# Optimization experiments

Hardware: AMD Instinct MI355X
Metric: run time of the kernel (lower is better)

The kernel has to match this reference:

```python
import jax, jax.numpy as jnp
import numpy as np

E, H, K = 768, 512, 8  # word_emb_size, nhidden, nhead
B, NA, NC = 32, 64, 64


def setup_inputs() -> dict:
    key = jax.random.key(0)
    ks = jax.random.split(key, 8)
    w = lambda k, shape: (jax.random.normal(k, shape, jnp.float32) * 0.02)
    return {
        'he_anchor': jax.random.normal(ks[0], (B, NA, E), jnp.float32),
        'he_pos': jax.random.normal(ks[1], (B, NC, E), jnp.float32),
        'he_neg': jax.random.uniform(ks[2], (B,), jnp.float32),  # SBERT target scores
        'Wa': w(ks[3], (H, E)), 'ba': jnp.zeros((H,), jnp.float32),
        'Wc': w(ks[4], (H, E)), 'bc': jnp.zeros((H,), jnp.float32),
        'Watt': w(ks[5], (K, H)), 'batt': jnp.zeros((K,), jnp.float32),
        'Wscore': w(ks[6], (1, K * H)), 'bscore': jnp.zeros((1,), jnp.float32),
    }


def _score(ha, hc, Wa, ba, Wc, bc, Watt, batt, Wscore, bscore):
    b, na, _ = ha.shape
    A = ha @ Wa.T + ba  # [B,Na,H]  (a2h)
    C = hc @ Wc.T + bc  # [B,Nc,H]  (c2h)
    # self_mul[b,i,j,h] = A[b,i,h]*C[b,j,h]; att logits = h2att(self_mul)
    logits = jnp.einsum('bih,bjh,kh->bkij', A, C, Watt) + batt[None, :, None, None]
    att = jax.nn.softmax(logits.reshape(b, K, -1), axis=-1).reshape(logits.shape)  # [B,K,Na,Nc]
    # per-head bilinear: out[b,k,h] = sum_ij A[b,i,h] * att[b,k,i,j] * C[b,j,h]
    out = jnp.einsum('bih,bkij,bjh->bkh', A, att, C)  # [B,K,H], head-major like torch cat
    score = out.reshape(b, K * H) @ Wscore.T + bscore  # [B,1]
    return score, att


def reference(he_anchor, he_pos, he_neg, Wa, ba, Wc, bc, Watt, batt, Wscore, bscore):
    score_p, att_map = _score(he_anchor, he_pos, Wa, ba, Wc, bc, Watt, batt, Wscore, bscore)
    score_bert = he_neg.reshape(-1, 1)
    loss = jnp.mean((score_p - score_bert) ** 2)  # nn.MSELoss
    return score_p, loss, att_map
```

## Files before the change

kernel.cpp:

```cpp
#include <hip/hip_runtime.h>

#define E_DIM 768

typedef __attribute__((ext_vector_type(8))) short bf16x8;
typedef __attribute__((ext_vector_type(4))) float f32x4;

__device__ __forceinline__ unsigned short f2bf(float f) {
    union { float f; unsigned int u; } v; v.f = f;
    unsigned int u = v.u;
    return (unsigned short)((u + 0x7FFFu + ((u >> 16) & 1u)) >> 16);
}
__device__ __forceinline__ float bfu_lo(unsigned int u) {
    union { unsigned int u; float f; } v; v.u = u << 16; return v.f;
}
__device__ __forceinline__ float bfu_hi(unsigned int u) {
    union { unsigned int u; float f; } v; v.u = u & 0xFFFF0000u; return v.f;
}
__device__ __forceinline__ unsigned int cvt_pk_bf16(float lo, float hi) {
    unsigned int u;
    asm("v_cvt_pk_bf16_f32 %0, %1, %2" : "=v"(u) : "v"(lo), "v"(hi));
    return u;
}

__global__ __launch_bounds__(256) void k_proj_mfma(
    const float* __restrict__ he_a, const float* __restrict__ Wa, const float* __restrict__ ba,
    const float* __restrict__ he_p, const float* __restrict__ Wc, const float* __restrict__ bc,
    unsigned short* __restrict__ dsts)
{
    __shared__ unsigned short Xs[128 * 40];
    __shared__ unsigned short Wl[64 * 40];
    int bid = blockIdx.x;
    int which = bid >> 7;
    int loc = bid & 127;
    int mbase = (loc >> 3) * 128;
    int hbase = (loc & 7) * 64;
    const float* Xg = which ? he_p : he_a;
    const float* Wg = which ? Wc : Wa;
    const float* bias = which ? bc : ba;
    int t = threadIdx.x;
    int lane = t & 63, w = t >> 6;
    int wr = w >> 1, wc = w & 1;

    float4 xr4[4];
    float4 wr4[2];
#pragma unroll
    for (int it = 0; it < 4; ++it) {
        int idx = t + it * 256; int row = idx >> 3, c4 = idx & 7;
        xr4[it] = *(const float4*)(Xg + (size_t)(mbase + row) * E_DIM + c4 * 4);
    }
#pragma unroll
    for (int it = 0; it < 2; ++it) {
        int idx = t + it * 256; int row = idx >> 3, c4 = idx & 7;
        wr4[it] = *(const float4*)(Wg + (size_t)(hbase + row) * E_DIM + c4 * 4);
    }

    f32x4 acc[4][2] = {};
    for (int kt = 0; kt < 24; ++kt) {
        __syncthreads();
#pragma unroll
        for (int it = 0; it < 4; ++it) {
            int idx = t + it * 256; int row = idx >> 3, c4 = idx & 7;
            uint2 u = make_uint2(cvt_pk_bf16(xr4[it].x, xr4[it].y),
                                 cvt_pk_bf16(xr4[it].z, xr4[it].w));
            *(uint2*)&Xs[row * 40 + c4 * 4] = u;
        }
#pragma unroll
        for (int it = 0; it < 2; ++it) {
            int idx = t + it * 256; int row = idx >> 3, c4 = idx & 7;
            uint2 u = make_uint2(cvt_pk_bf16(wr4[it].x, wr4[it].y),
                                 cvt_pk_bf16(wr4[it].z, wr4[it].w));
            *(uint2*)&Wl[row * 40 + c4 * 4] = u;
        }
        if (kt < 23) {
            int e0 = (kt + 1) * 32;
#pragma unroll
            for (int it = 0; it < 4; ++it) {
                int idx = t + it * 256; int row = idx >> 3, c4 = idx & 7;
                xr4[it] = *(const float4*)(Xg + (size_t)(mbase + row) * E_DIM + e0 + c4 * 4);
            }
#pragma unroll
            for (int it = 0; it < 2; ++it) {
                int idx = t + it * 256; int row = idx >> 3, c4 = idx & 7;
                wr4[it] = *(const float4*)(Wg + (size_t)(hbase + row) * E_DIM + e0 + c4 * 4);
            }
        }
        __syncthreads();
        int ar = lane & 15;
        int k0 = (lane >> 4) * 8;
        bf16x8 af[4], bfr[2];
#pragma unroll
        for (int mi = 0; mi < 4; ++mi)
            af[mi] = *(const bf16x8*)&Xs[(wr * 64 + mi * 16 + ar) * 40 + k0];
#pragma unroll
        for (int ni = 0; ni < 2; ++ni)
            bfr[ni] = *(const bf16x8*)&Wl[(wc * 32 + ni * 16 + ar) * 40 + k0];
#pragma unroll
        for (int mi = 0; mi < 4; ++mi)
#pragma unroll
            for (int ni = 0; ni < 2; ++ni)
                acc[mi][ni] = __builtin_amdgcn_mfma_f32_16x16x32_bf16(
                    af[mi], bfr[ni], acc[mi][ni], 0, 0, 0);
    }
#pragma unroll
    for (int ni = 0; ni < 2; ++ni) {
        int h = hbase + wc * 32 + ni * 16 + (lane & 15);
        float bv = bias[h];
#pragma unroll
        for (int mi = 0; mi < 4; ++mi) {
#pragma unroll
            for (int r = 0; r < 4; ++r) {
                int grow = mbase + wr * 64 + mi * 16 + (lane >> 4) * 4 + r;
                int b = grow >> 6, i = grow & 63;
                float v = acc[mi][ni][r] + bv;
                dsts[(size_t)b * 65536 + (which ? 32768 : 0) + i * 512 + h] = f2bf(v);
            }
        }
    }
}

__global__ __launch_bounds__(256) void k_att_mfma(
    float* __restrict__ out, const unsigned int* __restrict__ src,
    const float* __restrict__ Watt, const float* __restrict__ Wsc,
    float* __restrict__ partials)
{
    __shared__ unsigned short AkL[64 * 136];
    __shared__ unsigned short AgL[64 * 136];
    __shared__ unsigned short CL[64 * 136];
    __shared__ float WlK[512], WlG[512];
    __shared__ float red[4];
    int t = threadIdx.x;
    int lane = t & 63, w = t >> 6;
    int b = blockIdx.x & 31, k = blockIdx.x >> 5;
    const unsigned int* Au = src + (size_t)b * 32768;
    const unsigned int* Cu = Au + 16384;

    for (int s = t; s < 512; s += 256) {
        WlK[s] = Watt[k * 512 + s];
        WlG[s] = Wsc[k * 512 + s];
    }

    int row = t >> 2, seg = t & 3;
    const unsigned int* Arp = Au + row * 256 + seg * 16;
    const unsigned int* Crp = Cu + row * 256 + seg * 16;
    uint4 rA[4], rC[4];
#pragma unroll
    for (int g = 0; g < 4; ++g) {
        rA[g] = *(const uint4*)(Arp + g * 4);
        rC[g] = *(const uint4*)(Crp + g * 4);
    }
    __syncthreads();

    unsigned int* AkU = (unsigned int*)AkL;
    unsigned int* AgU = (unsigned int*)AgL;
    unsigned int* CU_ = (unsigned int*)CL;

    int arow = w * 16 + (lane & 15);
    int k0s = (lane >> 4) * 8;
    f32x4 accS[4] = {}, accG[4] = {};

    for (int c = 0; c < 4; ++c) {
        int hb = c * 128 + seg * 32;
#pragma unroll
        for (int g = 0; g < 4; ++g) {
            uint4 sv = rA[g];
            uint4 okv, ogv;
#pragma unroll
            for (int e = 0; e < 4; ++e) {
                unsigned int u = (&sv.x)[e];
                float a0 = bfu_lo(u), a1 = bfu_hi(u);
                int h0 = hb + (g * 4 + e) * 2;
                float2 wk = *(const float2*)&WlK[h0];
                float2 wg = *(const float2*)&WlG[h0];
                (&okv.x)[e] = cvt_pk_bf16(a0 * wk.x, a1 * wk.y);
                (&ogv.x)[e] = cvt_pk_bf16(a0 * wg.x, a1 * wg.y);
            }
            *(uint4*)&AkU[row * 68 + seg * 16 + g * 4] = okv;
            *(uint4*)&AgU[row * 68 + seg * 16 + g * 4] = ogv;
            *(uint4*)&CU_[row * 68 + seg * 16 + g * 4] = rC[g];
        }
        if (c < 3) {
#pragma unroll
            for (int g = 0; g < 4; ++g) {
                rA[g] = *(const uint4*)(Arp + (c + 1) * 64 + g * 4);
                rC[g] = *(const uint4*)(Crp + (c + 1) * 64 + g * 4);
            }
        }
        __syncthreads();
#pragma unroll
        for (int ks = 0; ks < 4; ++ks) {
            bf16x8 ak = *(const bf16x8*)&AkL[arow * 136 + ks * 32 + k0s];
            bf16x8 ag = *(const bf16x8*)&AgL[arow * 136 + ks * 32 + k0s];
#pragma unroll
            for (int ni = 0; ni < 4; ++ni) {
                bf16x8 cb = *(const bf16x8*)&CL[(ni * 16 + (lane & 15)) * 136 + ks * 32 + k0s];
                accS[ni] = __builtin_amdgcn_mfma_f32_16x16x32_bf16(ak, cb, accS[ni], 0, 0, 0);
                accG[ni] = __builtin_amdgcn_mfma_f32_16x16x32_bf16(ag, cb, accG[ni], 0, 0, 0);
            }
        }
        __syncthreads();
    }

    float lmax = accS[0][0];
#pragma unroll
    for (int ni = 0; ni < 4; ++ni)
#pragma unroll
        for (int r = 0; r < 4; ++r) lmax = fmaxf(lmax, accS[ni][r]);
    float v = lmax;
#pragma unroll
    for (int off = 32; off > 0; off >>= 1) v = fmaxf(v, __shfl_xor(v, off));
    if (lane == 0) red[w] = v;
    __syncthreads();
    float M = fmaxf(fmaxf(red[0], red[1]), fmaxf(red[2], red[3]));
    __syncthreads();
    float ev[16];
    float lsum = 0.f;
#pragma unroll
    for (int ni = 0; ni < 4; ++ni)
#pragma unroll
        for (int r = 0; r < 4; ++r) {
            float e = __expf(accS[ni][r] - M);
            ev[ni * 4 + r] = e;
            lsum += e;
        }
    v = lsum;
#pragma unroll
    for (int off = 32; off > 0; off >>= 1) v += __shfl_xor(v, off);
    if (lane == 0) red[w] = v;
    __syncthreads();
    float inv = 1.0f / (red[0] + red[1] + red[2] + red[3]);
    __syncthreads();
    float pacc = 0.f;
    float* attk = out + 33 + (size_t)b * 32768 + (size_t)k * 4096;
#pragma unroll
    for (int ni = 0; ni < 4; ++ni) {
        int j = ni * 16 + (lane & 15);
#pragma unroll
        for (int r = 0; r < 4; ++r) {
            int i = w * 16 + (lane >> 4) * 4 + r;
            float av = ev[ni * 4 + r] * inv;
            attk[i * 64 + j] = av;
            pacc += av * accG[ni][r];
        }
    }
    v = pacc;
#pragma unroll
    for (int off = 32; off > 0; off >>= 1) v += __shfl_xor(v, off);
    if (lane == 0) red[w] = v;
    __syncthreads();
    if (t == 0) partials[b * 8 + k] = red[0] + red[1] + red[2] + red[3];
}

__global__ __launch_bounds__(256) void k_att_valu8(
    float* __restrict__ out, const unsigned int* __restrict__ src,
    const float* __restrict__ Watt, const float* __restrict__ Wsc)
{
    __shared__ unsigned int Al[64 * 260];
    __shared__ unsigned int Cl[64 * 260];
    __shared__ float Wattl[512], Wscl[512];
    __shared__ float red[4];
    int t = threadIdx.x;
    int lane = t & 63, wave = t >> 6;
    int b = blockIdx.x;
    const unsigned int* srcb = src + (size_t)b * 32768;

    for (int s = t; s < 16384; s += 256) {
        int row = s >> 8, hp = s & 255;
        Al[row * 260 + hp] = srcb[s];
        Cl[row * 260 + hp] = srcb[16384 + s];
    }

    int i = t >> 2;
    int jb = (t & 3) * 16;
    float* attreg = out + 33 + (size_t)b * 32768;
    float blocktotal = 0.f;

    for (int k = 0; k < 8; ++k) {
        for (int s = t; s < 512; s += 256) {
            Wattl[s] = Watt[k * 512 + s];
            Wscl[s]  = Wsc[k * 512 + s];
        }
        __syncthreads();
        float sacc[16] = {}, gacc[16] = {};
        const unsigned int* Arow = &Al[i * 260];
        const unsigned int* Crow = &Cl[jb * 260];
        for (int hp = 0; hp < 256; hp += 2) {
            uint2 au = *(const uint2*)&Arow[hp];
            float a0 = bfu_lo(au.x), a1 = bfu_hi(au.x);
            float a2 = bfu_lo(au.y), a3 = bfu_hi(au.y);
            int h0 = hp * 2;
            float4 wk = *(const float4*)&Wattl[h0];
            float4 wg = *(const float4*)&Wscl[h0];
            float ak0 = a0 * wk.x, ak1 = a1 * wk.y, ak2 = a2 * wk.z, ak3 = a3 * wk.w;
            float ag0 = a0 * wg.x, ag1 = a1 * wg.y, ag2 = a2 * wg.z, ag3 = a3 * wg.w;
#pragma unroll
            for (int q = 0; q < 16; ++q) {
                uint2 cu = *(const uint2*)&Crow[q * 260 + hp];
                float c0 = bfu_lo(cu.x), c1 = bfu_hi(cu.x);
                float c2 = bfu_lo(cu.y), c3 = bfu_hi(cu.y);
                sacc[q] = fmaf(ak0, c0, sacc[q]); gacc[q] = fmaf(ag0, c0, gacc[q]);
                sacc[q] = fmaf(ak1, c1, sacc[q]); gacc[q] = fmaf(ag1, c1, gacc[q]);
                sacc[q] = fmaf(ak2, c2, sacc[q]); gacc[q] = fmaf(ag2, c2, gacc[q]);
                sacc[q] = fmaf(ak3, c3, sacc[q]); gacc[q] = fmaf(ag3, c3, gacc[q]);
            }
        }
        float lmax = sacc[0];
#pragma unroll
        for (int e = 1; e < 16; ++e) lmax = fmaxf(lmax, sacc[e]);
        float v = lmax;
#pragma unroll
        for (int off = 32; off > 0; off >>= 1) v = fmaxf(v, __shfl_xor(v, off));
        if (lane == 0) red[wave] = v;
        __syncthreads();
        float M = fmaxf(fmaxf(red[0], red[1]), fmaxf(red[2], red[3]));
        __syncthreads();
        float lsum = 0.f;
#pragma unroll
        for (int e = 0; e < 16; ++e) {
            sacc[e] = __expf(sacc[e] - M);
            lsum += sacc[e];
        }
        v = lsum;
#pragma unroll
        for (int off = 32; off > 0; off >>= 1) v += __shfl_xor(v, off);
        if (lane == 0) red[wave] = v;
        __syncthreads();
        float Z = red[0] + red[1] + red[2] + red[3];
        float inv = 1.0f / Z;
        __syncthreads();
        float pacc = 0.f;
        float* attk = attreg + k * 4096 + i * 64 + jb;
#pragma unroll
        for (int e = 0; e < 16; ++e) {
            float att = sacc[e] * inv;
            attk[e] = att;
            pacc += att * gacc[e];
        }
        v = pacc;
#pragma unroll
        for (int off = 32; off > 0; off >>= 1) v += __shfl_xor(v, off);
        if (lane == 0) red[wave] = v;
        __syncthreads();
        if (t == 0) blocktotal += red[0] + red[1] + red[2] + red[3];
        __syncthreads();
    }
    if (t == 0) out[b] = blocktotal;
}

__global__ __launch_bounds__(64) void k_loss(
    float* __restrict__ out, const float* __restrict__ he_neg,
    const float* __restrict__ partials, const float* __restrict__ bsc)
{
    __shared__ float sq[32];
    int t = threadIdx.x;
    if (t < 32) {
        float s;
        if (partials) {
            s = 0.f;
            for (int k = 0; k < 8; ++k) s += partials[t * 8 + k];
        } else {
            s = out[t];
        }
        s += bsc[0];
        out[t] = s;
        float d = s - he_neg[t];
        sq[t] = d * d;
    }
    __syncthreads();
    if (t == 0) {
        float l = 0.f;
        for (int i2 = 0; i2 < 32; ++i2) l += sq[i2];
        out[32] = l * (1.0f / 32.0f);
    }
}

extern "C" void kernel_launch(void* const* d_in, const int* in_sizes, int n_in,
                              void* d_out, int out_size, void* d_ws, size_t ws_size,
                              hipStream_t stream) {
    int iA = 0, iP = 1, iN = 2, iWa = 3, iBa = 4, iWc = 5, iBc = 6, iWatt = 7, iWsc = 9, iBsc = 10;
    if (!(in_sizes[0] == 1572864 && in_sizes[2] == 32)) {
        if (n_in == 11 && in_sizes[0] == 393216 && in_sizes[8] == 1572864) {
            iWa = 0; iWatt = 1; iWc = 2; iWsc = 3; iBa = 4; iBc = 6; iBsc = 7;
            iA = 8; iN = 9; iP = 10;
        }
    }
    const float* he_a  = (const float*)d_in[iA];
    const float* he_p  = (const float*)d_in[iP];
    const float* he_n  = (const float*)d_in[iN];
    const float* Wa    = (const float*)d_in[iWa];
    const float* ba    = (const float*)d_in[iBa];
    const float* Wc    = (const float*)d_in[iWc];
    const float* bc    = (const float*)d_in[iBc];
    const float* Watt  = (const float*)d_in[iWatt];
    const float* Wsc   = (const float*)d_in[iWsc];
    const float* bsc   = (const float*)d_in[iBsc];
    float* out = (float*)d_out;

    size_t need = ((size_t)4 << 20) + 4096;
    if (d_ws != nullptr && ws_size >= need) {
        unsigned short* wss = (unsigned short*)d_ws;
        float* partials = (float*)((char*)d_ws + ((size_t)4 << 20));
        k_proj_mfma<<<dim3(256), dim3(256), 0, stream>>>(he_a, Wa, ba, he_p, Wc, bc, wss);
        k_att_mfma<<<dim3(256), dim3(256), 0, stream>>>(out, (unsigned int*)wss, Watt, Wsc, partials);
        k_loss<<<dim3(1), dim3(64), 0, stream>>>(out, he_n, partials, bsc);
    } else {
        unsigned short* region = (unsigned short*)(out + 33);
        k_proj_mfma<<<dim3(256), dim3(256), 0, stream>>>(he_a, Wa, ba, he_p, Wc, bc, region);
        k_att_valu8<<<dim3(32), dim3(256), 0, stream>>>(out, (unsigned int*)region, Watt, Wsc);
        k_loss<<<dim3(1), dim3(64), 0, stream>>>(out, he_n, nullptr, bsc);
    }
}
```

Baseline: 49.96 us.

## Fuse loss into attention kernel via atomic counter and drop LDS staging

```diff
diff --git a/kernel.cpp b/kernel.cpp
--- a/kernel.cpp
+++ b/kernel.cpp
@@ -16,86 +16,74 @@
 __device__ __forceinline__ float bfu_hi(unsigned int u) {
     union { unsigned int u; float f; } v; v.u = u & 0xFFFF0000u; return v.f;
 }
+__device__ __forceinline__ float bfs(unsigned short s) {
+    union { unsigned int u; float f; } v; v.u = ((unsigned int)s) << 16; return v.f;
+}
 __device__ __forceinline__ unsigned int cvt_pk_bf16(float lo, float hi) {
     unsigned int u;
     asm("v_cvt_pk_bf16_f32 %0, %1, %2" : "=v"(u) : "v"(lo), "v"(hi));
     return u;
 }
 
-__global__ __launch_bounds__(256) void k_proj_mfma(
+__global__ __launch_bounds__(512) void k_proj_mfma(
     const float* __restrict__ he_a, const float* __restrict__ Wa, const float* __restrict__ ba,
     const float* __restrict__ he_p, const float* __restrict__ Wc, const float* __restrict__ bc,
-    unsigned short* __restrict__ dsts)
+    unsigned short* __restrict__ dsts, float* __restrict__ score_acc,
+    unsigned int* __restrict__ counter)
 {
     __shared__ unsigned short Xs[128 * 40];
     __shared__ unsigned short Wl[64 * 40];
+    int t = threadIdx.x;
     int bid = blockIdx.x;
+    if (bid == 0) {
+        if (t < 32) score_acc[t] = 0.f;
+        else if (t == 32) *counter = 0u;
+    }
     int which = bid >> 7;
     int loc = bid & 127;
-    int mbase = (loc >> 3) * 128;
-    int hbase = (loc & 7) * 64;
+    int mbase = (loc & 15) * 128;
+    int hbase = (loc >> 4) * 64;
     const float* Xg = which ? he_p : he_a;
     const float* Wg = which ? Wc : Wa;
     const float* bias = which ? bc : ba;
-    int t = threadIdx.x;
     int lane = t & 63, w = t >> 6;
     int wr = w >> 1, wc = w & 1;
 
-    float4 xr4[4];
-    float4 wr4[2];
-#pragma unroll
-    for (int it = 0; it < 4; ++it) {
-        int idx = t + it * 256; int row = idx >> 3, c4 = idx & 7;
-        xr4[it] = *(const float4*)(Xg + (size_t)(mbase + row) * E_DIM + c4 * 4);
-    }
-#pragma unroll
-    for (int it = 0; it < 2; ++it) {
-        int idx = t + it * 256; int row = idx >> 3, c4 = idx & 7;
-        wr4[it] = *(const float4*)(Wg + (size_t)(hbase + row) * E_DIM + c4 * 4);
-    }
-
-    f32x4 acc[4][2] = {};
+    int xr0 = t >> 3,          xc0 = t & 7;
+    int xr1 = (t + 512) >> 3,  xc1 = t & 7;
+    int wrr = t >> 3,          wcc = t & 7;
+
+    float4 p0 = *(const float4*)(Xg + (size_t)(mbase + xr0) * E_DIM + xc0 * 4);
+    float4 p1 = *(const float4*)(Xg + (size_t)(mbase + xr1) * E_DIM + xc1 * 4);
+    float4 p2 = *(const float4*)(Wg + (size_t)(hbase + wrr) * E_DIM + wcc * 4);
+
+    f32x4 acc[2][2] = {};
     for (int kt = 0; kt < 24; ++kt) {
         __syncthreads();
-#pragma unroll
-        for (int it = 0; it < 4; ++it) {
-            int idx = t + it * 256; int row = idx >> 3, c4 = idx & 7;
-            uint2 u = make_uint2(cvt_pk_bf16(xr4[it].x, xr4[it].y),
-                                 cvt_pk_bf16(xr4[it].z, xr4[it].w));
-            *(uint2*)&Xs[row * 40 + c4 * 4] = u;
-        }
-#pragma unroll
-        for (int it = 0; it < 2; ++it) {
-            int idx = t + it * 256; int row = idx >> 3, c4 = idx & 7;
-            uint2 u = make_uint2(cvt_pk_bf16(wr4[it].x, wr4[it].y),
-                                 cvt_pk_bf16(wr4[it].z, wr4[it].w));
-            *(uint2*)&Wl[row * 40 + c4 * 4] = u;
-        }
+        *(uint2*)&Xs[xr0 * 40 + xc0 * 4] =
+            make_uint2(cvt_pk_bf16(p0.x, p0.y), cvt_pk_bf16(p0.z, p0.w));
+        *(uint2*)&Xs[xr1 * 40 + xc1 * 4] =
+            make_uint2(cvt_pk_bf16(p1.x, p1.y), cvt_pk_bf16(p1.z, p1.w));
+        *(uint2*)&Wl[wrr * 40 + wcc * 4] =
+            make_uint2(cvt_pk_bf16(p2.x, p2.y), cvt_pk_bf16(p2.z, p2.w));
         if (kt < 23) {
             int e0 = (kt + 1) * 32;
-#pragma unroll
-            for (int it = 0; it < 4; ++it) {
-                int idx = t + it * 256; int row = idx >> 3, c4 = idx & 7;
-                xr4[it] = *(const float4*)(Xg + (size_t)(mbase + row) * E_DIM + e0 + c4 * 4);
-            }
-#pragma unroll
-            for (int it = 0; it < 2; ++it) {
-                int idx = t + it * 256; int row = idx >> 3, c4 = idx & 7;
-                wr4[it] = *(const float4*)(Wg + (size_t)(hbase + row) * E_DIM + e0 + c4 * 4);
-            }
+            p0 = *(const float4*)(Xg + (size_t)(mbase + xr0) * E_DIM + e0 + xc0 * 4);
+            p1 = *(const float4*)(Xg + (size_t)(mbase + xr1) * E_DIM + e0 + xc1 * 4);
+            p2 = *(const float4*)(Wg + (size_t)(hbase + wrr) * E_DIM + e0 + wcc * 4);
         }
         __syncthreads();
         int ar = lane & 15;
         int k0 = (lane >> 4) * 8;
-        bf16x8 af[4], bfr[2];
-#pragma unroll
-        for (int mi = 0; mi < 4; ++mi)
-            af[mi] = *(const bf16x8*)&Xs[(wr * 64 + mi * 16 + ar) * 40 + k0];
+        bf16x8 af[2], bfr[2];
+#pragma unroll
+        for (int mi = 0; mi < 2; ++mi)
+            af[mi] = *(const bf16x8*)&Xs[(wr * 32 + mi * 16 + ar) * 40 + k0];
 #pragma unroll
         for (int ni = 0; ni < 2; ++ni)
             bfr[ni] = *(const bf16x8*)&Wl[(wc * 32 + ni * 16 + ar) * 40 + k0];
 #pragma unroll
-        for (int mi = 0; mi < 4; ++mi)
+        for (int mi = 0; mi < 2; ++mi)
 #pragma unroll
             for (int ni = 0; ni < 2; ++ni)
                 acc[mi][ni] = __builtin_amdgcn_mfma_f32_16x16x32_bf16(
@@ -106,10 +94,10 @@
         int h = hbase + wc * 32 + ni * 16 + (lane & 15);
         float bv = bias[h];
 #pragma unroll
-        for (int mi = 0; mi < 4; ++mi) {
+        for (int mi = 0; mi < 2; ++mi) {
 #pragma unroll
             for (int r = 0; r < 4; ++r) {
-                int grow = mbase + wr * 64 + mi * 16 + (lane >> 4) * 4 + r;
+                int grow = mbase + wr * 32 + mi * 16 + (lane >> 4) * 4 + r;
                 int b = grow >> 6, i = grow & 63;
                 float v = acc[mi][ni][r] + bv;
                 dsts[(size_t)b * 65536 + (which ? 32768 : 0) + i * 512 + h] = f2bf(v);
@@ -118,91 +106,59 @@
     }
 }
 
-__global__ __launch_bounds__(256) void k_att_mfma(
-    float* __restrict__ out, const unsigned int* __restrict__ src,
+__global__ __launch_bounds__(512) void k_att_fused(
+    float* __restrict__ out, const unsigned short* __restrict__ src,
     const float* __restrict__ Watt, const float* __restrict__ Wsc,
-    float* __restrict__ partials)
+    const float* __restrict__ he_neg, const float* __restrict__ bsc,
+    float* __restrict__ score_acc, unsigned int* __restrict__ counter)
 {
-    __shared__ unsigned short AkL[64 * 136];
-    __shared__ unsigned short AgL[64 * 136];
-    __shared__ unsigned short CL[64 * 136];
-    __shared__ float WlK[512], WlG[512];
-    __shared__ float red[4];
+    __shared__ float red[8];
+    __shared__ float sqv[32];
+    __shared__ int lastflag;
     int t = threadIdx.x;
     int lane = t & 63, w = t >> 6;
+    int rf = w & 3, jh = w >> 2;
     int b = blockIdx.x & 31, k = blockIdx.x >> 5;
-    const unsigned int* Au = src + (size_t)b * 32768;
-    const unsigned int* Cu = Au + 16384;
-
-    for (int s = t; s < 512; s += 256) {
-        WlK[s] = Watt[k * 512 + s];
-        WlG[s] = Wsc[k * 512 + s];
-    }
-
-    int row = t >> 2, seg = t & 3;
-    const unsigned int* Arp = Au + row * 256 + seg * 16;
-    const unsigned int* Crp = Cu + row * 256 + seg * 16;
-    uint4 rA[4], rC[4];
-#pragma unroll
-    for (int g = 0; g < 4; ++g) {
-        rA[g] = *(const uint4*)(Arp + g * 4);
-        rC[g] = *(const uint4*)(Crp + g * 4);
-    }
-    __syncthreads();
-
-    unsigned int* AkU = (unsigned int*)AkL;
-    unsigned int* AgU = (unsigned int*)AgL;
-    unsigned int* CU_ = (unsigned int*)CL;
-
-    int arow = w * 16 + (lane & 15);
-    int k0s = (lane >> 4) * 8;
-    f32x4 accS[4] = {}, accG[4] = {};
-
-    for (int c = 0; c < 4; ++c) {
-        int hb = c * 128 + seg * 32;
-#pragma unroll
-        for (int g = 0; g < 4; ++g) {
-            uint4 sv = rA[g];
-            uint4 okv, ogv;
-#pragma unroll
-            for (int e = 0; e < 4; ++e) {
-                unsigned int u = (&sv.x)[e];
-                float a0 = bfu_lo(u), a1 = bfu_hi(u);
-                int h0 = hb + (g * 4 + e) * 2;
-                float2 wk = *(const float2*)&WlK[h0];
-                float2 wg = *(const float2*)&WlG[h0];
-                (&okv.x)[e] = cvt_pk_bf16(a0 * wk.x, a1 * wk.y);
-                (&ogv.x)[e] = cvt_pk_bf16(a0 * wg.x, a1 * wg.y);
-            }
-            *(uint4*)&AkU[row * 68 + seg * 16 + g * 4] = okv;
-            *(uint4*)&AgU[row * 68 + seg * 16 + g * 4] = ogv;
-            *(uint4*)&CU_[row * 68 + seg * 16 + g * 4] = rC[g];
-        }
-        if (c < 3) {
-#pragma unroll
-            for (int g = 0; g < 4; ++g) {
-                rA[g] = *(const uint4*)(Arp + (c + 1) * 64 + g * 4);
-                rC[g] = *(const uint4*)(Crp + (c + 1) * 64 + g * 4);
-            }
-        }
-        __syncthreads();
-#pragma unroll
-        for (int ks = 0; ks < 4; ++ks) {
-            bf16x8 ak = *(const bf16x8*)&AkL[arow * 136 + ks * 32 + k0s];
-            bf16x8 ag = *(const bf16x8*)&AgL[arow * 136 + ks * 32 + k0s];
-#pragma unroll
-            for (int ni = 0; ni < 4; ++ni) {
-                bf16x8 cb = *(const bf16x8*)&CL[(ni * 16 + (lane & 15)) * 136 + ks * 32 + k0s];
-                accS[ni] = __builtin_amdgcn_mfma_f32_16x16x32_bf16(ak, cb, accS[ni], 0, 0, 0);
-                accG[ni] = __builtin_amdgcn_mfma_f32_16x16x32_bf16(ag, cb, accG[ni], 0, 0, 0);
-            }
-        }
-        __syncthreads();
+    int l15 = lane & 15, lhi = lane >> 4;
+
+    const unsigned short* Ab = src + (size_t)b * 65536;
+    const unsigned short* Cb = Ab + 32768;
+    const unsigned short* ap  = Ab + (size_t)(rf * 16 + l15) * 512 + lhi * 8;
+    const unsigned short* cp0 = Cb + (size_t)(jh * 32 + l15) * 512 + lhi * 8;
+    const unsigned short* cp1 = cp0 + 16 * 512;
+    const float* wkbase = Watt + k * 512 + lhi * 8;
+    const float* wgbase = Wsc  + k * 512 + lhi * 8;
+
+    f32x4 accS[2] = {}, accG[2] = {};
+#pragma unroll 2
+    for (int ks = 0; ks < 16; ++ks) {
+        int h = ks * 32;
+        bf16x8 af  = *(const bf16x8*)(ap + h);
+        bf16x8 cb0 = *(const bf16x8*)(cp0 + h);
+        bf16x8 cb1 = *(const bf16x8*)(cp1 + h);
+        float wkv[8], wgv[8];
+        *(float4*)&wkv[0] = *(const float4*)(wkbase + h);
+        *(float4*)&wkv[4] = *(const float4*)(wkbase + h + 4);
+        *(float4*)&wgv[0] = *(const float4*)(wgbase + h);
+        *(float4*)&wgv[4] = *(const float4*)(wgbase + h + 4);
+        float a[8];
+#pragma unroll
+        for (int e = 0; e < 8; ++e) a[e] = bfs((unsigned short)af[e]);
+        union { unsigned int u[4]; bf16x8 v; } ak, ag;
+#pragma unroll
+        for (int e2 = 0; e2 < 4; ++e2) {
+            ak.u[e2] = cvt_pk_bf16(a[2 * e2] * wkv[2 * e2], a[2 * e2 + 1] * wkv[2 * e2 + 1]);
+            ag.u[e2] = cvt_pk_bf16(a[2 * e2] * wgv[2 * e2], a[2 * e2 + 1] * wgv[2 * e2 + 1]);
+        }
+        accS[0] = __builtin_amdgcn_mfma_f32_16x16x32_bf16(ak.v, cb0, accS[0], 0, 0, 0);
+        accS[1] = __builtin_amdgcn_mfma_f32_16x16x32_bf16(ak.v, cb1, accS[1], 0, 0, 0);
+        accG[0] = __builtin_amdgcn_mfma_f32_16x16x32_bf16(ag.v, cb0, accG[0], 0, 0, 0);
+        accG[1] = __builtin_amdgcn_mfma_f32_16x16x32_bf16(ag.v, cb1, accG[1], 0, 0, 0);
     }
 
     float lmax = accS[0][0];
 #pragma unroll
-    for (int ni = 0; ni < 4; ++ni)
+    for (int ni = 0; ni < 2; ++ni)
 #pragma unroll
         for (int r = 0; r < 4; ++r) lmax = fmaxf(lmax, accS[ni][r]);
     float v = lmax;
@@ -210,12 +166,14 @@
     for (int off = 32; off > 0; off >>= 1) v = fmaxf(v, __shfl_xor(v, off));
     if (lane == 0) red[w] = v;
     __syncthreads();
-    float M = fmaxf(fmaxf(red[0], red[1]), fmaxf(red[2], red[3]));
-    __syncthreads();
-    float ev[16];
+    float M = red[0];
+#pragma unroll
+    for (int q = 1; q < 8; ++q) M = fmaxf(M, red[q]);
+    __syncthreads();
+    float ev[8];
     float lsum = 0.f;
 #pragma unroll
-    for (int ni = 0; ni < 4; ++ni)
+    for (int ni = 0; ni < 2; ++ni)
 #pragma unroll
         for (int r = 0; r < 4; ++r) {
             float e = __expf(accS[ni][r] - M);
@@ -227,16 +185,20 @@
     for (int off = 32; off > 0; off >>= 1) v += __shfl_xor(v, off);
     if (lane == 0) red[w] = v;
     __syncthreads();
-    float inv = 1.0f / (red[0] + red[1] + red[2] + red[3]);
-    __syncthreads();
+    float Z = 0.f;
+#pragma unroll
+    for (int q = 0; q < 8; ++q) Z += red[q];
+    float inv = 1.0f / Z;
+    __syncthreads();
+
     float pacc = 0.f;
     float* attk = out + 33 + (size_t)b * 32768 + (size_t)k * 4096;
 #pragma unroll
-    for (int ni = 0; ni < 4; ++ni) {
-        int j = ni * 16 + (lane & 15);
+    for (int ni = 0; ni < 2; ++ni) {
+        int j = jh * 32 + ni * 16 + l15;
 #pragma unroll
         for (int r = 0; r < 4; ++r) {
-            int i = w * 16 + (lane >> 4) * 4 + r;
+            int i = rf * 16 + lhi * 4 + r;
             float av = ev[ni * 4 + r] * inv;
             attk[i * 64 + j] = av;
             pacc += av * accG[ni][r];
@@ -247,7 +209,31 @@
     for (int off = 32; off > 0; off >>= 1) v += __shfl_xor(v, off);
     if (lane == 0) red[w] = v;
     __syncthreads();
-    if (t == 0) partials[b * 8 + k] = red[0] + red[1] + red[2] + red[3];
+    if (t == 0) {
+        float tot = 0.f;
+#pragma unroll
+        for (int q = 0; q < 8; ++q) tot += red[q];
+        atomicAdd(&score_acc[b], tot);
+        __threadfence();
+        unsigned int done = atomicAdd(counter, 1u);
+        lastflag = (done == 255u) ? 1 : 0;
+    }
+    __syncthreads();
+    if (lastflag) {
+        __threadfence();
+        if (t < 32) {
+            float s = atomicAdd(&score_acc[t], 0.0f) + bsc[0];
+            out[t] = s;
+            float d = s - he_neg[t];
+            sqv[t] = d * d;
+        }
+        __syncthreads();
+        if (t == 0) {
+            float l = 0.f;
+            for (int q = 0; q < 32; ++q) l += sqv[q];
+            out[32] = l * (1.0f / 32.0f);
+        }
+    }
 }
 
 __global__ __launch_bounds__(256) void k_att_valu8(
@@ -348,19 +334,12 @@
 
 __global__ __launch_bounds__(64) void k_loss(
     float* __restrict__ out, const float* __restrict__ he_neg,
-    const float* __restrict__ partials, const float* __restrict__ bsc)
+    const float* __restrict__ bsc)
 {
     __shared__ float sq[32];
     int t = threadIdx.x;
     if (t < 32) {
-        float s;
-        if (partials) {
-            s = 0.f;
-            for (int k = 0; k < 8; ++k) s += partials[t * 8 + k];
-        } else {
-            s = out[t];
-        }
-        s += bsc[0];
+        float s = out[t] + bsc[0];
         out[t] = s;
         float d = s - he_neg[t];
         sq[t] = d * d;
@@ -395,17 +374,22 @@
     const float* bsc   = (const float*)d_in[iBsc];
     float* out = (float*)d_out;
 
-    size_t need = ((size_t)4 << 20) + 4096;
+    size_t need = ((size_t)4 << 20) + 256;
     if (d_ws != nullptr && ws_size >= need) {
         unsigned short* wss = (unsigned short*)d_ws;
-        float* partials = (float*)((char*)d_ws + ((size_t)4 << 20));
-        k_proj_mfma<<<dim3(256), dim3(256), 0, stream>>>(he_a, Wa, ba, he_p, Wc, bc, wss);
-        k_att_mfma<<<dim3(256), dim3(256), 0, stream>>>(out, (unsigned int*)wss, Watt, Wsc, partials);
-        k_loss<<<dim3(1), dim3(64), 0, stream>>>(out, he_n, partials, bsc);
+        float* score_acc = (float*)((char*)d_ws + ((size_t)4 << 20));
+        unsigned int* counter = (unsigned int*)(score_acc + 32);
+        k_proj_mfma<<<dim3(256), dim3(512), 0, stream>>>(
+            he_a, Wa, ba, he_p, Wc, bc, wss, score_acc, counter);
+        k_att_fused<<<dim3(256), dim3(512), 0, stream>>>(
+            out, wss, Watt, Wsc, he_n, bsc, score_acc, counter);
     } else {
         unsigned short* region = (unsigned short*)(out + 33);
-        k_proj_mfma<<<dim3(256), dim3(256), 0, stream>>>(he_a, Wa, ba, he_p, Wc, bc, region);
+        static float s_dummy[33];
+        (void)s_dummy;
+        k_proj_mfma<<<dim3(256), dim3(512), 0, stream>>>(
+            he_a, Wa, ba, he_p, Wc, bc, region, (float*)(out), (unsigned int*)(out + 32));
         k_att_valu8<<<dim3(32), dim3(256), 0, stream>>>(out, (unsigned int*)region, Watt, Wsc);
-        k_loss<<<dim3(1), dim3(64), 0, stream>>>(out, he_n, nullptr, bsc);
-    }
-}
+        k_loss<<<dim3(1), dim3(64), 0, stream>>>(out, he_n, bsc);
+    }
+}
```

After: 51.05 us. 1.02x slower.
